# Kernel tuning notes

Hardware: AMD Instinct MI355X
Metric: run time of the kernel (lower is better)

The kernel has to match this reference:

```python
import jax, jax.numpy as jnp
import numpy as np

B, N_IN, N_OUT = 8192, 2048, 2048


def setup_inputs() -> dict:
    key = jax.random.key(0)
    kx, kw = jax.random.split(key)
    x = jax.random.normal(kx, (B, N_IN), dtype=jnp.float32)
    # torch: uniform_(-0.5, 0.5)
    weight = jax.random.uniform(kw, (N_IN, N_OUT), dtype=jnp.float32, minval=-0.5, maxval=0.5)
    return {"x": x, "weight": weight}


def reference(x, weight):
    # Binarize: W > 0 -> {0, 1}; then dense matmul (batch, n_in) @ (n_in, n_out)
    w_bin = (weight > 0).astype(x.dtype)
    return x @ w_bin
```

## Files before the change

kernel.cpp:

```cpp
#include <hip/hip_runtime.h>


#define MDIM 8192
#define NDIM 2048
#define KDIM 2048
#define NT   (KDIM / 128)
#define CH   (64 * KDIM)

typedef __attribute__((ext_vector_type(8))) short short8;
typedef __attribute__((ext_vector_type(4))) float float4v;
typedef __attribute__((ext_vector_type(4))) float f32x4;
typedef __attribute__((ext_vector_type(4))) int int4v;
typedef __attribute__((ext_vector_type(4))) unsigned short ushort4v;
typedef __attribute__((ext_vector_type(8))) unsigned short ushort8v;

__device__ __forceinline__ unsigned short f2bf(float f) {
    union { float f; unsigned u; } v; v.f = f;
    unsigned r = v.u + 0x7FFFu + ((v.u >> 16) & 1u);
    return (unsigned short)(r >> 16);
}

__device__ __forceinline__ void gload_lds16(void* l, const void* g) {
    __builtin_amdgcn_global_load_lds(
        (const __attribute__((address_space(1))) unsigned int*)g,
        (__attribute__((address_space(3))) unsigned int*)l,
        16, 0, 0);
}

#define FENCE asm volatile("" ::: "memory")
#define BAR do { FENCE; __builtin_amdgcn_s_barrier(); FENCE; } while (0)

__global__ __launch_bounds__(256) void cvt_xq(const float* __restrict__ X,
                                              signed char* __restrict__ Xq,
                                              float* __restrict__ Sc) {
    const int row = blockIdx.x;
    const int t = threadIdx.x;
    const float* xr = X + (size_t)row * KDIM + t * 8;
    float4v a = *reinterpret_cast<const float4v*>(xr);
    float4v b = *reinterpret_cast<const float4v*>(xr + 4);
    float m = fabsf(a[0]);
    m = fmaxf(m, fabsf(a[1])); m = fmaxf(m, fabsf(a[2])); m = fmaxf(m, fabsf(a[3]));
    m = fmaxf(m, fabsf(b[0])); m = fmaxf(m, fabsf(b[1]));
    m = fmaxf(m, fabsf(b[2])); m = fmaxf(m, fabsf(b[3]));
#pragma unroll
    for (int off = 32; off; off >>= 1)
        m = fmaxf(m, __shfl_xor(m, off));
    __shared__ float wm[4];
    if ((t & 63) == 0) wm[t >> 6] = m;
    __syncthreads();
    const float s = fmaxf(fmaxf(wm[0], wm[1]), fmaxf(wm[2], wm[3]));
    const float inv = (s > 0.f) ? 127.0f / s : 0.f;

    int q[8];
    q[0] = __float2int_rn(a[0] * inv); q[1] = __float2int_rn(a[1] * inv);
    q[2] = __float2int_rn(a[2] * inv); q[3] = __float2int_rn(a[3] * inv);
    q[4] = __float2int_rn(b[0] * inv); q[5] = __float2int_rn(b[1] * inv);
    q[6] = __float2int_rn(b[2] * inv); q[7] = __float2int_rn(b[3] * inv);
    unsigned lo = (q[0] & 255) | ((q[1] & 255) << 8) | ((q[2] & 255) << 16) | ((unsigned)(q[3] & 255) << 24);
    unsigned hi = (q[4] & 255) | ((q[5] & 255) << 8) | ((q[6] & 255) << 16) | ((unsigned)(q[7] & 255) << 24);
    unsigned* dst = (unsigned*)(Xq + (size_t)row * KDIM + t * 8);
    dst[0] = lo; dst[1] = hi;
    if (t == 0) Sc[row] = s * (1.0f / 127.0f);
}

__global__ __launch_bounds__(256) void bin_w8(const float* __restrict__ W,
                                              signed char* __restrict__ Wt) {
    __shared__ __align__(16) signed char T[64][80];
    const int t = threadIdx.x;
    const int k0 = (blockIdx.x >> 5) * 64;
    const int n0 = (blockIdx.x & 31) * 64;
    const int kr = t >> 4;
    const int nc = (t & 15) * 4;
#pragma unroll
    for (int rr = 0; rr < 4; ++rr) {
        int k = k0 + rr * 16 + kr;
        float4v w4 = *reinterpret_cast<const float4v*>(W + (size_t)k * NDIM + n0 + nc);
#pragma unroll
        for (int c = 0; c < 4; ++c)
            T[nc + c][rr * 16 + kr] = (w4[c] > 0.0f) ? (signed char)1 : (signed char)0;
    }
    __syncthreads();
    const int row = t >> 2, ch = t & 3;
    int4v v = *reinterpret_cast<const int4v*>(&T[row][ch * 16]);
    *reinterpret_cast<int4v*>(Wt + (size_t)(n0 + row) * KDIM + k0 + ch * 16) = v;
}

__global__ __launch_bounds__(512, 1) void gemm_i8(const signed char* __restrict__ A,
                                                  const signed char* __restrict__ Bt,
                                                  const float* __restrict__ Sc,
                                                  float* __restrict__ O) {
    extern __shared__ char lds[];
    const int tid  = threadIdx.x;
    const int lane = tid & 63;
    const int w    = tid >> 6;
    const int wr   = w >> 2;
    const int wc   = w & 3;

    int id  = blockIdx.x;
    int swz = (id & 7) * 32 + (id >> 3);
    const int bm = swz >> 3;
    const int bn = swz & 7;

    const int l3 = lane >> 3, l7 = lane & 7;
    const int srcOff = (w * 8 + l3) * KDIM + ((l7 ^ l3) << 4);
    const char* gA = (const char*)A + (size_t)(bm * 256) * KDIM + srcOff;
    const char* gB = (const char*)Bt + (size_t)(bn * 256) * KDIM + srcOff;

    const int fr = lane & 15, fg = lane >> 4;
    const int se0 = ((fg)     ^ (fr & 7)) << 4;
    const int se1 = ((4 + fg) ^ (fr & 7)) << 4;
    const int aRd = (wr * 128 + fr) * 128;
    const int bRd = 32768 + (wc * 64 + fr) * 128;

    int4v acc[8][4];
#pragma unroll
    for (int i = 0; i < 8; ++i)
#pragma unroll
        for (int j = 0; j < 4; ++j) {
            acc[i][j][0] = 0; acc[i][j][1] = 0; acc[i][j][2] = 0; acc[i][j][3] = 0;
        }

    gload_lds16(lds + 32768 + 0 * 8192 + w * 1024, gB + 0 * CH);
    gload_lds16(lds + 32768 + 2 * 8192 + w * 1024, gB + 2 * CH);
    gload_lds16(lds + 32768 + 1 * 8192 + w * 1024, gB + 1 * CH);
    gload_lds16(lds + 32768 + 3 * 8192 + w * 1024, gB + 3 * CH);
    gload_lds16(lds + 0 * 8192 + w * 1024, gA + 0 * CH);
    gload_lds16(lds + 2 * 8192 + w * 1024, gA + 2 * CH);
    gload_lds16(lds + 1 * 8192 + w * 1024, gA + 1 * CH);
    gload_lds16(lds + 3 * 8192 + w * 1024, gA + 3 * CH);
    asm volatile("s_waitcnt vmcnt(0)" ::: "memory");
    BAR;

    int4v af[4], bfr[4];

    for (int t = 0; t < NT; ++t) {
        const int cur = (t & 1) << 16;
        const int nxt = ((t + 1) & 1) << 16;
        const bool more = (t + 1 < NT);
        const char* gAs = gA + (size_t)(t + 1) * 128;
        const char* gBs = gB + (size_t)(t + 1) * 128;

        asm volatile("s_waitcnt vmcnt(2)" ::: "memory");
        BAR;
#pragma unroll
        for (int j = 0; j < 4; ++j)
            af[j] = *reinterpret_cast<const int4v*>(lds + cur + aRd + j * 2048 + se0);
#pragma unroll
        for (int n = 0; n < 4; ++n)
            bfr[n] = *reinterpret_cast<const int4v*>(lds + cur + bRd + n * 2048 + se0);
        if (more) {
            gload_lds16(lds + nxt + 32768 + 0 * 8192 + w * 1024, gBs + 0 * CH);
            gload_lds16(lds + nxt + 32768 + 2 * 8192 + w * 1024, gBs + 2 * CH);
        }
        __builtin_amdgcn_s_setprio(1);
#pragma unroll
        for (int mi = 0; mi < 4; ++mi)
#pragma unroll
            for (int ni = 0; ni < 4; ++ni)
                acc[mi][ni] = __builtin_amdgcn_mfma_i32_16x16x64_i8(
                    af[mi], bfr[ni], acc[mi][ni], 0, 0, 0);
        __builtin_amdgcn_s_setprio(0);

        if (more) asm volatile("s_waitcnt vmcnt(2)" ::: "memory");
        else      asm volatile("s_waitcnt vmcnt(0)" ::: "memory");
        BAR;
#pragma unroll
        for (int j = 0; j < 4; ++j)
            af[j] = *reinterpret_cast<const int4v*>(lds + cur + aRd + (4 + j) * 2048 + se0);
        if (more) {
            gload_lds16(lds + nxt + 32768 + 1 * 8192 + w * 1024, gBs + 1 * CH);
            gload_lds16(lds + nxt + 32768 + 3 * 8192 + w * 1024, gBs + 3 * CH);
        }
        __builtin_amdgcn_s_setprio(1);
#pragma unroll
        for (int mi = 0; mi < 4; ++mi)
#pragma unroll
            for (int ni = 0; ni < 4; ++ni)
                acc[4 + mi][ni] = __builtin_amdgcn_mfma_i32_16x16x64_i8(
                    af[mi], bfr[ni], acc[4 + mi][ni], 0, 0, 0);
        __builtin_amdgcn_s_setprio(0);

        BAR;
#pragma unroll
        for (int j = 0; j < 4; ++j)
            af[j] = *reinterpret_cast<const int4v*>(lds + cur + aRd + j * 2048 + se1);
#pragma unroll
        for (int n = 0; n < 4; ++n)
            bfr[n] = *reinterpret_cast<const int4v*>(lds + cur + bRd + n * 2048 + se1);
        if (more) {
            gload_lds16(lds + nxt + 0 * 8192 + w * 1024, gAs + 0 * CH);
            gload_lds16(lds + nxt + 2 * 8192 + w * 1024, gAs + 2 * CH);
        }
        __builtin_amdgcn_s_setprio(1);
#pragma unroll
        for (int mi = 0; mi < 4; ++mi)
#pragma unroll
            for (int ni = 0; ni < 4; ++ni)
                acc[mi][ni] = __builtin_amdgcn_mfma_i32_16x16x64_i8(
                    af[mi], bfr[ni], acc[mi][ni], 0, 0, 0);
        __builtin_amdgcn_s_setprio(0);

        BAR;
#pragma unroll
        for (int j = 0; j < 4; ++j)
            af[j] = *reinterpret_cast<const int4v*>(lds + cur + aRd + (4 + j) * 2048 + se1);
        if (more) {
            gload_lds16(lds + nxt + 1 * 8192 + w * 1024, gAs + 1 * CH);
            gload_lds16(lds + nxt + 3 * 8192 + w * 1024, gAs + 3 * CH);
        }
        __builtin_amdgcn_s_setprio(1);
#pragma unroll
        for (int mi = 0; mi < 4; ++mi)
#pragma unroll
            for (int ni = 0; ni < 4; ++ni)
                acc[4 + mi][ni] = __builtin_amdgcn_mfma_i32_16x16x64_i8(
                    af[mi], bfr[ni], acc[4 + mi][ni], 0, 0, 0);
        __builtin_amdgcn_s_setprio(0);
    }

    const int orow0 = bm * 256 + wr * 128 + fg * 4;
    const int ocol0 = bn * 256 + wc * 64 + fr;
#pragma unroll
    for (int mi = 0; mi < 8; ++mi)
#pragma unroll
        for (int r = 0; r < 4; ++r) {
            const int row = orow0 + mi * 16 + r;
            const float s = Sc[row];
            float* op = O + (size_t)row * NDIM + ocol0;
#pragma unroll
            for (int ni = 0; ni < 4; ++ni)
                op[ni * 16] = s * (float)acc[mi][ni][r];
        }
}

__global__ __launch_bounds__(256, 2) void binlin_fused(
        const float* __restrict__ X, const float* __restrict__ W,
        float* __restrict__ O) {
    const int tid = threadIdx.x;
    const int lane = tid & 63;
    const int wave = tid >> 6;
    const int wr = wave >> 1, wc = wave & 1;
    const int NWG = (MDIM / 128) * (NDIM / 128);
    int id = blockIdx.x;
    int swz = (id & 7) * (NWG >> 3) + (id >> 3);
    const int bm = swz >> 4, bn = swz & 15;

    __shared__ __align__(16) unsigned short As[128][40];
    __shared__ __align__(16) unsigned short Bs[128][40];

    const int rA = tid >> 3, kA = (tid & 7) * 4;
    const float* aPtr = X + (size_t)(bm * 128 + rA) * KDIM + kA;
    const int nB = (tid & 31) * 4, kB = (tid >> 5) * 4;
    const float* bPtr = W + (size_t)kB * NDIM + (size_t)bn * 128 + nB;

    float4v aReg[4], bReg[4];
#pragma unroll
    for (int p = 0; p < 4; ++p)
        aReg[p] = *reinterpret_cast<const float4v*>(aPtr + (size_t)(32 * p) * KDIM);
#pragma unroll
    for (int dk = 0; dk < 4; ++dk)
        bReg[dk] = *reinterpret_cast<const float4v*>(bPtr + (size_t)dk * NDIM);

    f32x4 acc[4][4];
#pragma unroll
    for (int i = 0; i < 4; ++i)
#pragma unroll
        for (int j = 0; j < 4; ++j) {
            acc[i][j][0] = 0.f; acc[i][j][1] = 0.f; acc[i][j][2] = 0.f; acc[i][j][3] = 0.f;
        }

    const int r16 = lane & 15, g8 = (lane >> 4) * 8;
    for (int kt = 0; kt < KDIM; kt += 32) {
#pragma unroll
        for (int p = 0; p < 4; ++p) {
            ushort4v v;
            v[0] = f2bf(aReg[p][0]); v[1] = f2bf(aReg[p][1]);
            v[2] = f2bf(aReg[p][2]); v[3] = f2bf(aReg[p][3]);
            *reinterpret_cast<ushort4v*>(&As[rA + 32 * p][kA]) = v;
        }
        unsigned short bb[4][4];
#pragma unroll
        for (int dk = 0; dk < 4; ++dk)
#pragma unroll
            for (int dn = 0; dn < 4; ++dn)
                bb[dn][dk] = (bReg[dk][dn] > 0.0f) ? (unsigned short)0x3F80u
                                                   : (unsigned short)0u;
#pragma unroll
        for (int dn = 0; dn < 4; ++dn) {
            ushort4v v;
            v[0] = bb[dn][0]; v[1] = bb[dn][1]; v[2] = bb[dn][2]; v[3] = bb[dn][3];
            *reinterpret_cast<ushort4v*>(&Bs[nB + dn][kB]) = v;
        }
        __syncthreads();
        if (kt + 32 < KDIM) {
#pragma unroll
            for (int p = 0; p < 4; ++p)
                aReg[p] = *reinterpret_cast<const float4v*>(
                    aPtr + (size_t)(32 * p) * KDIM + (kt + 32));
#pragma unroll
            for (int dk = 0; dk < 4; ++dk)
                bReg[dk] = *reinterpret_cast<const float4v*>(
                    bPtr + (size_t)(kt + 32 + dk) * NDIM);
        }
        short8 af[4], bf[4];
#pragma unroll
        for (int mi = 0; mi < 4; ++mi)
            af[mi] = *reinterpret_cast<const short8*>(&As[wr * 64 + mi * 16 + r16][g8]);
#pragma unroll
        for (int ni = 0; ni < 4; ++ni)
            bf[ni] = *reinterpret_cast<const short8*>(&Bs[wc * 64 + ni * 16 + r16][g8]);
#pragma unroll
        for (int mi = 0; mi < 4; ++mi)
#pragma unroll
            for (int ni = 0; ni < 4; ++ni)
                acc[mi][ni] = __builtin_amdgcn_mfma_f32_16x16x32_bf16(
                    af[mi], bf[ni], acc[mi][ni], 0, 0, 0);
        __syncthreads();
    }

    const int orow0 = bm * 128 + wr * 64 + (lane >> 4) * 4;
    const int ocol0 = bn * 128 + wc * 64 + r16;
#pragma unroll
    for (int mi = 0; mi < 4; ++mi)
#pragma unroll
        for (int ni = 0; ni < 4; ++ni)
#pragma unroll
            for (int r = 0; r < 4; ++r)
                O[(size_t)(orow0 + mi * 16 + r) * NDIM + ocol0 + ni * 16] =
                    acc[mi][ni][r];
}

extern "C" void kernel_launch(void* const* d_in, const int* in_sizes, int n_in,
                              void* d_out, int out_size, void* d_ws, size_t ws_size,
                              hipStream_t stream) {
    const float* X = (const float*)d_in[0];
    const float* W = (const float*)d_in[1];
    float* O = (float*)d_out;
    (void)in_sizes; (void)n_in; (void)out_size;

    const size_t xq_bytes = (size_t)MDIM * KDIM;
    const size_t wt_bytes = (size_t)NDIM * KDIM;
    const size_t sc_bytes = (size_t)MDIM * sizeof(float);
    const size_t need = xq_bytes + wt_bytes + sc_bytes;

    if (ws_size >= need) {
        signed char* Xq = (signed char*)d_ws;
        signed char* Wt = Xq + xq_bytes;
        float* Sc = (float*)(Wt + wt_bytes);
        hipFuncSetAttribute((const void*)gemm_i8,
                            hipFuncAttributeMaxDynamicSharedMemorySize, 131072);
        cvt_xq<<<dim3(MDIM), dim3(256), 0, stream>>>(X, Xq, Sc);
        bin_w8<<<dim3((KDIM / 64) * (NDIM / 64)), dim3(256), 0, stream>>>(W, Wt);
        gemm_i8<<<dim3((MDIM / 256) * (NDIM / 256)), dim3(512), 131072, stream>>>(Xq, Wt, Sc, O);
    } else {
        binlin_fused<<<dim3((MDIM / 128) * (NDIM / 128)), dim3(256), 0, stream>>>(X, W, O);
    }
}
```

Measured before the change: 57.36 us.

## Merge prep kernels and restructure GEMM main loop into two phases per K tile

The activation quantization kernel and the weight binarize/transpose kernel are merged into one launch, with blocks split by index, which removes a launch and lets the two phases overlap. In the int8 GEMM, each K tile now loads both k-halves of the fragments at once and issues two MFMAs per accumulator. This halves the barriers per tile (four down to two) and batches the global-to-LDS prefetches into two groups of four. The cost is higher register pressure from doubled fragment arrays and less interleaving between the prefetch loads and the compute.

```diff
diff --git a/kernel.cpp b/kernel.cpp
--- a/kernel.cpp
+++ b/kernel.cpp
@@ -30,59 +30,62 @@
 #define FENCE asm volatile("" ::: "memory")
 #define BAR do { FENCE; __builtin_amdgcn_s_barrier(); FENCE; } while (0)
 
-__global__ __launch_bounds__(256) void cvt_xq(const float* __restrict__ X,
-                                              signed char* __restrict__ Xq,
-                                              float* __restrict__ Sc) {
-    const int row = blockIdx.x;
+__global__ __launch_bounds__(256) void prep(const float* __restrict__ X,
+                                            const float* __restrict__ W,
+                                            signed char* __restrict__ Xq,
+                                            signed char* __restrict__ Wt,
+                                            float* __restrict__ Sc) {
+    __shared__ __align__(16) signed char T[64][80];
+    __shared__ float wm[4];
     const int t = threadIdx.x;
-    const float* xr = X + (size_t)row * KDIM + t * 8;
-    float4v a = *reinterpret_cast<const float4v*>(xr);
-    float4v b = *reinterpret_cast<const float4v*>(xr + 4);
-    float m = fabsf(a[0]);
-    m = fmaxf(m, fabsf(a[1])); m = fmaxf(m, fabsf(a[2])); m = fmaxf(m, fabsf(a[3]));
-    m = fmaxf(m, fabsf(b[0])); m = fmaxf(m, fabsf(b[1]));
-    m = fmaxf(m, fabsf(b[2])); m = fmaxf(m, fabsf(b[3]));
-#pragma unroll
-    for (int off = 32; off; off >>= 1)
-        m = fmaxf(m, __shfl_xor(m, off));
-    __shared__ float wm[4];
-    if ((t & 63) == 0) wm[t >> 6] = m;
-    __syncthreads();
-    const float s = fmaxf(fmaxf(wm[0], wm[1]), fmaxf(wm[2], wm[3]));
-    const float inv = (s > 0.f) ? 127.0f / s : 0.f;
-
-    int q[8];
-    q[0] = __float2int_rn(a[0] * inv); q[1] = __float2int_rn(a[1] * inv);
-    q[2] = __float2int_rn(a[2] * inv); q[3] = __float2int_rn(a[3] * inv);
-    q[4] = __float2int_rn(b[0] * inv); q[5] = __float2int_rn(b[1] * inv);
-    q[6] = __float2int_rn(b[2] * inv); q[7] = __float2int_rn(b[3] * inv);
-    unsigned lo = (q[0] & 255) | ((q[1] & 255) << 8) | ((q[2] & 255) << 16) | ((unsigned)(q[3] & 255) << 24);
-    unsigned hi = (q[4] & 255) | ((q[5] & 255) << 8) | ((q[6] & 255) << 16) | ((unsigned)(q[7] & 255) << 24);
-    unsigned* dst = (unsigned*)(Xq + (size_t)row * KDIM + t * 8);
-    dst[0] = lo; dst[1] = hi;
-    if (t == 0) Sc[row] = s * (1.0f / 127.0f);
-}
-
-__global__ __launch_bounds__(256) void bin_w8(const float* __restrict__ W,
-                                              signed char* __restrict__ Wt) {
-    __shared__ __align__(16) signed char T[64][80];
-    const int t = threadIdx.x;
-    const int k0 = (blockIdx.x >> 5) * 64;
-    const int n0 = (blockIdx.x & 31) * 64;
-    const int kr = t >> 4;
-    const int nc = (t & 15) * 4;
-#pragma unroll
-    for (int rr = 0; rr < 4; ++rr) {
-        int k = k0 + rr * 16 + kr;
-        float4v w4 = *reinterpret_cast<const float4v*>(W + (size_t)k * NDIM + n0 + nc);
-#pragma unroll
-        for (int c = 0; c < 4; ++c)
-            T[nc + c][rr * 16 + kr] = (w4[c] > 0.0f) ? (signed char)1 : (signed char)0;
+    const int bid = blockIdx.x;
+
+    if (bid < MDIM) {
+        const int row = bid;
+        const float* xr = X + (size_t)row * KDIM + t * 8;
+        float4v a = *reinterpret_cast<const float4v*>(xr);
+        float4v b = *reinterpret_cast<const float4v*>(xr + 4);
+        float m = fabsf(a[0]);
+        m = fmaxf(m, fabsf(a[1])); m = fmaxf(m, fabsf(a[2])); m = fmaxf(m, fabsf(a[3]));
+        m = fmaxf(m, fabsf(b[0])); m = fmaxf(m, fabsf(b[1]));
+        m = fmaxf(m, fabsf(b[2])); m = fmaxf(m, fabsf(b[3]));
+#pragma unroll
+        for (int off = 32; off; off >>= 1)
+            m = fmaxf(m, __shfl_xor(m, off));
+        if ((t & 63) == 0) wm[t >> 6] = m;
+        __syncthreads();
+        const float s = fmaxf(fmaxf(wm[0], wm[1]), fmaxf(wm[2], wm[3]));
+        const float inv = (s > 0.f) ? 127.0f / s : 0.f;
+
+        int q[8];
+        q[0] = __float2int_rn(a[0] * inv); q[1] = __float2int_rn(a[1] * inv);
+        q[2] = __float2int_rn(a[2] * inv); q[3] = __float2int_rn(a[3] * inv);
+        q[4] = __float2int_rn(b[0] * inv); q[5] = __float2int_rn(b[1] * inv);
+        q[6] = __float2int_rn(b[2] * inv); q[7] = __float2int_rn(b[3] * inv);
+        unsigned lo = (q[0] & 255) | ((q[1] & 255) << 8) | ((q[2] & 255) << 16) | ((unsigned)(q[3] & 255) << 24);
+        unsigned hi = (q[4] & 255) | ((q[5] & 255) << 8) | ((q[6] & 255) << 16) | ((unsigned)(q[7] & 255) << 24);
+        unsigned* dst = (unsigned*)(Xq + (size_t)row * KDIM + t * 8);
+        dst[0] = lo; dst[1] = hi;
+        if (t == 0) Sc[row] = s * (1.0f / 127.0f);
+    } else {
+        const int wb = bid - MDIM;
+        const int k0 = (wb >> 5) * 64;
+        const int n0 = (wb & 31) * 64;
+        const int kr = t >> 4;
+        const int nc = (t & 15) * 4;
+#pragma unroll
+        for (int rr = 0; rr < 4; ++rr) {
+            int k = k0 + rr * 16 + kr;
+            float4v w4 = *reinterpret_cast<const float4v*>(W + (size_t)k * NDIM + n0 + nc);
+#pragma unroll
+            for (int c = 0; c < 4; ++c)
+                T[nc + c][rr * 16 + kr] = (w4[c] > 0.0f) ? (signed char)1 : (signed char)0;
+        }
+        __syncthreads();
+        const int row = t >> 2, ch = t & 3;
+        int4v v = *reinterpret_cast<const int4v*>(&T[row][ch * 16]);
+        *reinterpret_cast<int4v*>(Wt + (size_t)(n0 + row) * KDIM + k0 + ch * 16) = v;
     }
-    __syncthreads();
-    const int row = t >> 2, ch = t & 3;
-    int4v v = *reinterpret_cast<const int4v*>(&T[row][ch * 16]);
-    *reinterpret_cast<int4v*>(Wt + (size_t)(n0 + row) * KDIM + k0 + ch * 16) = v;
 }
 
 __global__ __launch_bounds__(512, 1) void gemm_i8(const signed char* __restrict__ A,
@@ -131,7 +134,7 @@
     asm volatile("s_waitcnt vmcnt(0)" ::: "memory");
     BAR;
 
-    int4v af[4], bfr[4];
+    int4v af[4][2], bfr[4][2];
 
     for (int t = 0; t < NT; ++t) {
         const int cur = (t & 1) << 16;
@@ -143,68 +146,44 @@
         asm volatile("s_waitcnt vmcnt(2)" ::: "memory");
         BAR;
 #pragma unroll
-        for (int j = 0; j < 4; ++j)
-            af[j] = *reinterpret_cast<const int4v*>(lds + cur + aRd + j * 2048 + se0);
-#pragma unroll
-        for (int n = 0; n < 4; ++n)
-            bfr[n] = *reinterpret_cast<const int4v*>(lds + cur + bRd + n * 2048 + se0);
+        for (int j = 0; j < 4; ++j) {
+            af[j][0] = *reinterpret_cast<const int4v*>(lds + cur + aRd + j * 2048 + se0);
+            af[j][1] = *reinterpret_cast<const int4v*>(lds + cur + aRd + j * 2048 + se1);
+        }
+#pragma unroll
+        for (int n = 0; n < 4; ++n) {
+            bfr[n][0] = *reinterpret_cast<const int4v*>(lds + cur + bRd + n * 2048 + se0);
+            bfr[n][1] = *reinterpret_cast<const int4v*>(lds + cur + bRd + n * 2048 + se1);
+        }
         if (more) {
             gload_lds16(lds + nxt + 32768 + 0 * 8192 + w * 1024, gBs + 0 * CH);
             gload_lds16(lds + nxt + 32768 + 2 * 8192 + w * 1024, gBs + 2 * CH);
+            gload_lds16(lds + nxt + 32768 + 1 * 8192 + w * 1024, gBs + 1 * CH);
+            gload_lds16(lds + nxt + 32768 + 3 * 8192 + w * 1024, gBs + 3 * CH);
         }
         __builtin_amdgcn_s_setprio(1);
 #pragma unroll
         for (int mi = 0; mi < 4; ++mi)
 #pragma unroll
-            for (int ni = 0; ni < 4; ++ni)
+            for (int ni = 0; ni < 4; ++ni) {
                 acc[mi][ni] = __builtin_amdgcn_mfma_i32_16x16x64_i8(
-                    af[mi], bfr[ni], acc[mi][ni], 0, 0, 0);
+                    af[mi][0], bfr[ni][0], acc[mi][ni], 0, 0, 0);
+                acc[mi][ni] = __builtin_amdgcn_mfma_i32_16x16x64_i8(
+                    af[mi][1], bfr[ni][1], acc[mi][ni], 0, 0, 0);
+            }
         __builtin_amdgcn_s_setprio(0);
 
-        if (more) asm volatile("s_waitcnt vmcnt(2)" ::: "memory");
+        if (more) asm volatile("s_waitcnt vmcnt(4)" ::: "memory");
         else      asm volatile("s_waitcnt vmcnt(0)" ::: "memory");
         BAR;
 #pragma unroll
-        for (int j = 0; j < 4; ++j)
-            af[j] = *reinterpret_cast<const int4v*>(lds + cur + aRd + (4 + j) * 2048 + se0);
-        if (more) {
-            gload_lds16(lds + nxt + 32768 + 1 * 8192 + w * 1024, gBs + 1 * CH);
-            gload_lds16(lds + nxt + 32768 + 3 * 8192 + w * 1024, gBs + 3 * CH);
-        }
-        __builtin_amdgcn_s_setprio(1);
-#pragma unroll
-        for (int mi = 0; mi < 4; ++mi)
-#pragma unroll
-            for (int ni = 0; ni < 4; ++ni)
-                acc[4 + mi][ni] = __builtin_amdgcn_mfma_i32_16x16x64_i8(
-                    af[mi], bfr[ni], acc[4 + mi][ni], 0, 0, 0);
-        __builtin_amdgcn_s_setprio(0);
-
-        BAR;
-#pragma unroll
-        for (int j = 0; j < 4; ++j)
-            af[j] = *reinterpret_cast<const int4v*>(lds + cur + aRd + j * 2048 + se1);
-#pragma unroll
-        for (int n = 0; n < 4; ++n)
-            bfr[n] = *reinterpret_cast<const int4v*>(lds + cur + bRd + n * 2048 + se1);
+        for (int j = 0; j < 4; ++j) {
+            af[j][0] = *reinterpret_cast<const int4v*>(lds + cur + aRd + (4 + j) * 2048 + se0);
+            af[j][1] = *reinterpret_cast<const int4v*>(lds + cur + aRd + (4 + j) * 2048 + se1);
+        }
         if (more) {
             gload_lds16(lds + nxt + 0 * 8192 + w * 1024, gAs + 0 * CH);
             gload_lds16(lds + nxt + 2 * 8192 + w * 1024, gAs + 2 * CH);
-        }
-        __builtin_amdgcn_s_setprio(1);
-#pragma unroll
-        for (int mi = 0; mi < 4; ++mi)
-#pragma unroll
-            for (int ni = 0; ni < 4; ++ni)
-                acc[mi][ni] = __builtin_amdgcn_mfma_i32_16x16x64_i8(
-                    af[mi], bfr[ni], acc[mi][ni], 0, 0, 0);
-        __builtin_amdgcn_s_setprio(0);
-
-        BAR;
-#pragma unroll
-        for (int j = 0; j < 4; ++j)
-            af[j] = *reinterpret_cast<const int4v*>(lds + cur + aRd + (4 + j) * 2048 + se1);
-        if (more) {
             gload_lds16(lds + nxt + 1 * 8192 + w * 1024, gAs + 1 * CH);
             gload_lds16(lds + nxt + 3 * 8192 + w * 1024, gAs + 3 * CH);
         }
@@ -212,9 +191,12 @@
 #pragma unroll
         for (int mi = 0; mi < 4; ++mi)
 #pragma unroll
-            for (int ni = 0; ni < 4; ++ni)
+            for (int ni = 0; ni < 4; ++ni) {
                 acc[4 + mi][ni] = __builtin_amdgcn_mfma_i32_16x16x64_i8(
-                    af[mi], bfr[ni], acc[4 + mi][ni], 0, 0, 0);
+                    af[mi][0], bfr[ni][0], acc[4 + mi][ni], 0, 0, 0);
+                acc[4 + mi][ni] = __builtin_amdgcn_mfma_i32_16x16x64_i8(
+                    af[mi][1], bfr[ni][1], acc[4 + mi][ni], 0, 0, 0);
+            }
         __builtin_amdgcn_s_setprio(0);
     }
 
@@ -349,8 +331,7 @@
         float* Sc = (float*)(Wt + wt_bytes);
         hipFuncSetAttribute((const void*)gemm_i8,
                             hipFuncAttributeMaxDynamicSharedMemorySize, 131072);
-        cvt_xq<<<dim3(MDIM), dim3(256), 0, stream>>>(X, Xq, Sc);
-        bin_w8<<<dim3((KDIM / 64) * (NDIM / 64)), dim3(256), 0, stream>>>(W, Wt);
+        prep<<<dim3(MDIM + (KDIM / 64) * (NDIM / 64)), dim3(256), 0, stream>>>(X, W, Xq, Wt, Sc);
         gemm_i8<<<dim3((MDIM / 256) * (NDIM / 256)), dim3(512), 131072, stream>>>(Xq, Wt, Sc, O);
     } else {
         binlin_fused<<<dim3((MDIM / 128) * (NDIM / 128)), dim3(256), 0, stream>>>(X, W, O);
```

Result: faster. 55.80 us (-2.7%).
